# Performance work log

Hardware: AMD Instinct MI355X
Metric: run time of the kernel (lower is better)

The kernel has to match this reference:

```python
import jax, jax.numpy as jnp
import numpy as np

N_NODES = 50000
N_NEIB = 64
D = 256
BATCH = 1024
N_SAMPLES = (25, 10)  # fanout per layer (layer_specs n_sample)


def setup_inputs() -> dict:
    key = jax.random.key(0)
    ks = jax.random.split(key, 12)
    inp = {
        'ids': jax.random.randint(ks[0], (BATCH,), 0, N_NODES),
        'diff_idx': jax.random.randint(ks[1], (N_NODES, N_NEIB), 0, N_NODES),
        'diff_val': jax.random.uniform(ks[2], (N_NODES, N_NEIB), dtype=jnp.float32),
        'feats': jax.random.normal(ks[3], (N_NODES, D), dtype=jnp.float32),
    }
    # two aggregator layers, each: fc_x, fc_neib : D -> D (= output_dim//2)
    for li in range(2):
        inp[f'Wx{li+1}'] = jax.random.normal(ks[4 + 4 * li], (D, D), dtype=jnp.float32) * 0.05
        inp[f'bx{li+1}'] = jnp.zeros((D,), dtype=jnp.float32)
        inp[f'Wn{li+1}'] = jax.random.normal(ks[5 + 4 * li], (D, D), dtype=jnp.float32) * 0.05
        inp[f'bn{li+1}'] = jnp.zeros((D,), dtype=jnp.float32)
    return inp


def _sample(diff_idx, diff_val, ids, n_samples, key):
    # gather candidate neighbor rows, shared random column permutation, take first n_samples
    tmp_idx = diff_idx[ids]            # [n, N_NEIB]
    tmp_val = diff_val[ids]
    perm = jax.random.permutation(key, tmp_idx.shape[1])
    idx = tmp_idx[:, perm][:, :n_samples].reshape(-1)
    val = tmp_val[:, perm][:, :n_samples].reshape(-1)
    return idx, val


def _agg(x, neib, vals, Wx, bx, Wn, bn):
    # weighted-mean neighbor aggregation + self/neib linear combine + relu
    n = x.shape[0]
    d = neib.shape[1]
    neib = neib.reshape(n, -1, d)              # [n, s, d]
    vals = vals.reshape(n, -1)                 # [n, s]
    w = vals / (jnp.sum(vals, axis=1, keepdims=True) + 1e-10)
    m = jnp.einsum('nsd,ns->nd', neib, w)      # weighted mean of neighbors
    return jax.nn.relu(x @ Wx + bx + m @ Wn + bn)


def reference(ids, diff_idx, diff_val, feats,
              Wx1, bx1, Wn1, bn1, Wx2, bx2, Wn2, bn2):
    skey = jax.random.key(42)
    all_feats = [feats[ids]]
    all_vals = []
    cur = ids
    for li, n in enumerate(N_SAMPLES):
        cur, vals = _sample(diff_idx, diff_val, cur, n, jax.random.fold_in(skey, li))
        all_feats.append(feats[cur])
        all_vals.append(vals)
    params = [(Wx1, bx1, Wn1, bn1), (Wx2, bx2, Wn2, bn2)]
    for Wx, bx, Wn, bn in params:
        all_feats = [_agg(all_feats[k], all_feats[k + 1], all_vals[k], Wx, bx, Wn, bn)
                     for k in range(len(all_feats) - 1)]
    assert len(all_feats) == 1
    return all_feats[0]  # [BATCH, D]
```

## Files before the change

### kernel.cpp

```cpp
#include <hip/hip_runtime.h>
#include <stdint.h>
#include <stddef.h>
#include <algorithm>

#define BATCH  1024
#define S1     25
#define S2     10
#define DIM    256
#define NNEIB  64
#define L2ROWS (BATCH * S1)
#define MROWS  (BATCH + BATCH * S1)
#define KTOT   512
#define NFEAT  50000

struct Perm25 { int p[S1]; };
struct Perm10 { int p[S2]; };

typedef __attribute__((ext_vector_type(8))) short short8;
typedef __attribute__((ext_vector_type(4))) float f32x4;

static inline uint32_t rotl_(uint32_t x, int d) { return (x << d) | (x >> (32 - d)); }

static void tf2x32(uint32_t k0, uint32_t k1, uint32_t x0, uint32_t x1,
                   uint32_t* o0, uint32_t* o1) {
  const uint32_t ks0 = k0, ks1 = k1, ks2 = k0 ^ k1 ^ 0x1BD11BDAu;
  static const int R[8] = {13, 15, 26, 6, 17, 29, 16, 24};
  x0 += ks0; x1 += ks1;
  for (int g = 0; g < 5; ++g) {
    const int* rr = R + (g & 1) * 4;
    for (int i = 0; i < 4; i++) { x0 += x1; x1 = rotl_(x1, rr[i]); x1 ^= x0; }
    uint32_t a, b;
    switch (g) {
      default:
      case 0: a = ks1; b = ks2; break;
      case 1: a = ks2; b = ks0; break;
      case 2: a = ks0; b = ks1; break;
      case 3: a = ks1; b = ks2; break;
      case 4: a = ks2; b = ks0; break;
    }
    x0 += a; x1 = x1 + b + (uint32_t)(g + 1);
  }
  *o0 = x0; *o1 = x1;
}

static void compute_perm(uint32_t li, int n, int* out) {
  uint32_t k0, k1, s0, s1;
  tf2x32(0u, 42u, 0u, li, &k0, &k1);
  tf2x32(k0, k1, 0u, 1u, &s0, &s1);
  uint32_t bits[NNEIB];
  for (int i = 0; i < NNEIB; i++) {
    uint32_t a, b;
    tf2x32(s0, s1, 0u, (uint32_t)i, &a, &b);
    bits[i] = a ^ b;
  }
  int idx[NNEIB];
  for (int i = 0; i < NNEIB; i++) idx[i] = i;
  std::stable_sort(idx, idx + NNEIB, [&](int A, int B) { return bits[A] < bits[B]; });
  for (int j = 0; j < n; j++) out[j] = idx[j];
}

__device__ __forceinline__ unsigned short f2bf(float x) {
  union { float f; uint32_t u; } v; v.f = x;
  uint32_t r = (v.u + 0x7FFFu + ((v.u >> 16) & 1u)) >> 16;
  return (unsigned short)r;
}
__device__ __forceinline__ float bfbits2f(uint32_t lo16) {
  union { uint32_t u; float f; } v; v.u = lo16 << 16;
  return v.f;
}
__device__ __forceinline__ void gload16(const unsigned short* g, unsigned short* l) {
  __builtin_amdgcn_global_load_lds(
      (const __attribute__((address_space(1))) unsigned int*)g,
      (__attribute__((address_space(3))) unsigned int*)l, 16, 0, 0);
}


#define PREP_CONVF   12500
#define PREP_CONVW   512
#define PREP_BLOCKS  (PREP_CONVF + 2 * PREP_CONVW + 4)
__global__ __launch_bounds__(256) void prep_k(
    const float* __restrict__ feats, uint32_t* __restrict__ fb,
    const float* __restrict__ Wx1, const float* __restrict__ Wn1,
    unsigned short* __restrict__ Wt1,
    const float* __restrict__ Wx2, const float* __restrict__ Wn2,
    unsigned short* __restrict__ Wt2,
    const int* __restrict__ ids, const int* __restrict__ dix,
    const float* __restrict__ dval, int* __restrict__ idx1,
    float* __restrict__ w1, Perm25 pm) {
  int b = blockIdx.x, t = threadIdx.x;
  if (b < PREP_CONVF) {
    int i = b * 256 + t;
    f32x4 v = *(const f32x4*)&feats[(size_t)i * 4];
    uint2 o;
    o.x = f2bf(v.x) | ((uint32_t)f2bf(v.y) << 16);
    o.y = f2bf(v.z) | ((uint32_t)f2bf(v.w) << 16);
    ((uint2*)fb)[i] = o;
  } else if (b < PREP_CONVF + 2 * PREP_CONVW) {
    int wi = b - PREP_CONVF;
    const float* Wx = (wi < PREP_CONVW) ? Wx1 : Wx2;
    const float* Wn = (wi < PREP_CONVW) ? Wn1 : Wn2;
    unsigned short* Wt = (wi < PREP_CONVW) ? Wt1 : Wt2;
    int idx = (wi % PREP_CONVW) * 256 + t;
    int n = idx >> 9, k = idx & 511;
    float v = (k < DIM) ? Wx[(size_t)k * DIM + n] : Wn[(size_t)(k - DIM) * DIM + n];
    Wt[(size_t)n * KTOT + k] = f2bf(v);
  } else {
    int i = (b - PREP_CONVF - 2 * PREP_CONVW) * 256 + t;
    if (i >= BATCH) return;
    int nid = ids[i];
    const float* vr = dval + (size_t)nid * NNEIB;
    const int* ir = dix + (size_t)nid * NNEIB;
    float v[S1];
    float s = 0.f;
    for (int j = 0; j < S1; j++) { v[j] = vr[pm.p[j]]; s += v[j]; }
    float inv = 1.f / (s + 1e-10f);
    for (int j = 0; j < S1; j++) {
      w1[i * S1 + j] = v[j] * inv;
      idx1[i * S1 + j] = ir[pm.p[j]];
    }
  }
}

template <int S>
__device__ __forceinline__ void agg_pairs(const uint4* __restrict__ fb, int nbl,
                                          float wl, int lane, float a[8]) {
  int h = lane >> 5, l5 = lane & 31;
#pragma unroll
  for (int p = 0; p < (S + 1) / 2; p++) {
    int jj = 2 * p + h;
    int nid = __shfl(nbl, (jj < S) ? jj : 0);
    float wj = (jj < S) ? __shfl(wl, jj) : 0.f;
    uint4 u = fb[(size_t)nid * 32 + l5];
    a[0] += wj * bfbits2f(u.x & 0xffffu); a[1] += wj * bfbits2f(u.x >> 16);
    a[2] += wj * bfbits2f(u.y & 0xffffu); a[3] += wj * bfbits2f(u.y >> 16);
    a[4] += wj * bfbits2f(u.z & 0xffffu); a[5] += wj * bfbits2f(u.z >> 16);
    a[6] += wj * bfbits2f(u.w & 0xffffu); a[7] += wj * bfbits2f(u.w >> 16);
  }
}

__global__ __launch_bounds__(256) void stage1_k(
    const uint4* __restrict__ fb, const int* __restrict__ idx1,
    const float* __restrict__ w1, const int* __restrict__ dix,
    const float* __restrict__ dval, Perm10 pm2, uint4* __restrict__ M1) {
  int wave = threadIdx.x >> 6, lane = threadIdx.x & 63;
  int r = blockIdx.x * 4 + wave;
  float a[8] = {0.f, 0.f, 0.f, 0.f, 0.f, 0.f, 0.f, 0.f};
  if (r < BATCH) {
    int nbl = 0; float wl = 0.f;
    if (lane < S1) { nbl = idx1[r * S1 + lane]; wl = w1[r * S1 + lane]; }
    agg_pairs<S1>(fb, nbl, wl, lane, a);
  } else {
    int nx = idx1[r - BATCH];
    int nbl = 0; float vj = 0.f;
    if (lane < S2) {
      int c = pm2.p[lane];
      nbl = dix[(size_t)nx * NNEIB + c];
      vj = dval[(size_t)nx * NNEIB + c];
    }
    float tot = 0.f;
#pragma unroll
    for (int j = 0; j < S2; j++) tot += __shfl(vj, j);
    float wl = vj / (tot + 1e-10f);
    agg_pairs<S2>(fb, nbl, wl, lane, a);
  }
#pragma unroll
  for (int q = 0; q < 8; q++) a[q] += __shfl_xor(a[q], 32);
  if (lane < 32) {
    uint4 o;
    o.x = f2bf(a[0]) | ((uint32_t)f2bf(a[1]) << 16);
    o.y = f2bf(a[2]) | ((uint32_t)f2bf(a[3]) << 16);
    o.z = f2bf(a[4]) | ((uint32_t)f2bf(a[5]) << 16);
    o.w = f2bf(a[6]) | ((uint32_t)f2bf(a[7]) << 16);
    M1[(size_t)r * 32 + (lane & 31)] = o;
  }
}

__global__ __launch_bounds__(256) void stage2_k(
    const uint2* __restrict__ Hb, const float* __restrict__ w1,
    uint2* __restrict__ M2) {
  int wave = threadIdx.x >> 6, lane = threadIdx.x & 63;
  int i = blockIdx.x * 4 + wave;
  float wl = (lane < S1) ? w1[(size_t)i * S1 + lane] : 0.f;
  const uint2* hb = Hb + (size_t)(BATCH + i * S1) * 64 + lane;
  float a0 = 0.f, a1 = 0.f, a2 = 0.f, a3 = 0.f;
#pragma unroll
  for (int j = 0; j < S1; j++) {
    float wj = __shfl(wl, j);
    uint2 u = hb[(size_t)j * 64];
    a0 += wj * bfbits2f(u.x & 0xffffu);
    a1 += wj * bfbits2f(u.x >> 16);
    a2 += wj * bfbits2f(u.y & 0xffffu);
    a3 += wj * bfbits2f(u.y >> 16);
  }
  uint2 o;
  o.x = f2bf(a0) | ((uint32_t)f2bf(a1) << 16);
  o.y = f2bf(a2) | ((uint32_t)f2bf(a3) << 16);
  M2[(size_t)i * 64 + lane] = o;
}

#define BK 32
template <int TBM, int TBN, bool OUT_BF16, bool GATHER>
__global__ __launch_bounds__(256) void gemm_k(
    const unsigned short* __restrict__ Ax, const int* __restrict__ ids,
    const int* __restrict__ idx1, const unsigned short* __restrict__ Am,
    const unsigned short* __restrict__ Wt, const float* __restrict__ bx,
    const float* __restrict__ bn, void* __restrict__ OutP) {
  constexpr int MI = TBM / 32;
  constexpr int NJ = TBN / 32;
  __shared__ __align__(16) unsigned short As[TBM][BK];
  __shared__ __align__(16) unsigned short Bs[TBN][BK];
  int t = threadIdx.x;
  int wave = t >> 6, lane = t & 63, quad = lane >> 4, l16 = lane & 15;
  int wm = (wave >> 1) * (TBM / 2);
  int wn = (wave & 1) * (TBN / 2);
  int row0 = blockIdx.x * TBM, col0 = blockIdx.y * TBN;

  f32x4 acc[MI][NJ];
#pragma unroll
  for (int i = 0; i < MI; i++)
#pragma unroll
    for (int j = 0; j < NJ; j++) acc[i][j] = (f32x4){0.f, 0.f, 0.f, 0.f};

  int rl = lane >> 2;
  int cl = (lane & 3) * 8;

  const unsigned short* xsrc[TBM / 64];
  const unsigned short* msrc[TBM / 64];
#pragma unroll
  for (int c = 0; c < TBM / 64; c++) {
    int grow = row0 + c * 64 + wave * 16 + rl;
    int xr = GATHER ? ((grow < BATCH) ? ids[grow] : idx1[grow - BATCH]) : grow;
    xsrc[c] = Ax + (size_t)xr * DIM + cl;
    msrc[c] = Am + (size_t)grow * DIM + cl - DIM;
  }

  for (int k0 = 0; k0 < KTOT; k0 += BK) {
#pragma unroll
    for (int c = 0; c < TBM / 64; c++)
      gload16(((k0 < DIM) ? xsrc[c] : msrc[c]) + k0, &As[c * 64 + wave * 16][0]);
#pragma unroll
    for (int c = 0; c < TBN / 64; c++) {
      int row = c * 64 + wave * 16 + rl;
      gload16(Wt + (size_t)(col0 + row) * KTOT + k0 + cl, &Bs[c * 64 + wave * 16][0]);
    }
    __syncthreads();

    short8 af[MI], bfr[NJ];
#pragma unroll
    for (int i = 0; i < MI; i++)
      af[i] = *(const short8*)&As[wm + i * 16 + l16][quad * 8];
#pragma unroll
    for (int j = 0; j < NJ; j++)
      bfr[j] = *(const short8*)&Bs[wn + j * 16 + l16][quad * 8];
#pragma unroll
    for (int i = 0; i < MI; i++)
#pragma unroll
      for (int j = 0; j < NJ; j++)
        acc[i][j] = __builtin_amdgcn_mfma_f32_16x16x32_bf16(af[i], bfr[j], acc[i][j], 0, 0, 0);
    __syncthreads();
  }

  float bias[NJ];
#pragma unroll
  for (int j = 0; j < NJ; j++) {
    int c = col0 + wn + j * 16 + l16;
    bias[j] = bx[c] + bn[c];
  }
#pragma unroll
  for (int i = 0; i < MI; i++) {
#pragma unroll
    for (int j = 0; j < NJ; j++) {
      int c = col0 + wn + j * 16 + l16;
#pragma unroll
      for (int reg = 0; reg < 4; reg++) {
        int r = row0 + wm + i * 16 + quad * 4 + reg;
        float v = fmaxf(acc[i][j][reg] + bias[j], 0.f);
        if (OUT_BF16)
          ((unsigned short*)OutP)[(size_t)r * DIM + c] = f2bf(v);
        else
          ((float*)OutP)[(size_t)r * DIM + c] = v;
      }
    }
  }
}

static inline size_t align256(size_t x) { return (x + 255) & ~(size_t)255; }

extern "C" void kernel_launch(void* const* d_in, const int* in_sizes, int n_in,
                              void* d_out, int out_size, void* d_ws, size_t ws_size,
                              hipStream_t stream) {
  const int*   ids  = (const int*)d_in[0];
  const int*   dix  = (const int*)d_in[1];
  const float* dval = (const float*)d_in[2];
  const float* feats= (const float*)d_in[3];
  const float* Wx1  = (const float*)d_in[4];
  const float* bx1  = (const float*)d_in[5];
  const float* Wn1  = (const float*)d_in[6];
  const float* bn1  = (const float*)d_in[7];
  const float* Wx2  = (const float*)d_in[8];
  const float* bx2  = (const float*)d_in[9];
  const float* Wn2  = (const float*)d_in[10];
  const float* bn2  = (const float*)d_in[11];
  float* out = (float*)d_out;

  Perm25 p25;
  Perm10 p10;
  compute_perm(0u, S1, p25.p);
  compute_perm(1u, S2, p10.p);

  char* w = (char*)d_ws;
  int*            idx1 = (int*)w;            w += align256(sizeof(int) * L2ROWS);
  float*          w1   = (float*)w;          w += align256(sizeof(float) * L2ROWS);
  uint32_t*       fb   = (uint32_t*)w;       w += align256(2 * (size_t)NFEAT * DIM);
  unsigned short* M1   = (unsigned short*)w; w += align256(2 * (size_t)MROWS * DIM);
  unsigned short* Hb   = (unsigned short*)w; w += align256(2 * (size_t)MROWS * DIM);
  unsigned short* M2   = (unsigned short*)w; w += align256(2 * (size_t)BATCH * DIM);
  unsigned short* Wt1  = (unsigned short*)w; w += align256(2 * (size_t)DIM * KTOT);
  unsigned short* Wt2  = (unsigned short*)w; w += align256(2 * (size_t)DIM * KTOT);

  prep_k<<<PREP_BLOCKS, 256, 0, stream>>>(feats, fb, Wx1, Wn1, Wt1, Wx2, Wn2, Wt2,
                                          ids, dix, dval, idx1, w1, p25);
  stage1_k<<<MROWS / 4, 256, 0, stream>>>((const uint4*)fb, idx1, w1, dix, dval, p10,
                                          (uint4*)M1);
  gemm_k<128, 128, true, true><<<dim3(MROWS / 128, DIM / 128), 256, 0, stream>>>(
      (const unsigned short*)fb, ids, idx1, M1, Wt1, bx1, bn1, Hb);
  stage2_k<<<BATCH / 4, 256, 0, stream>>>((const uint2*)Hb, w1, (uint2*)M2);
  gemm_k<64, 64, false, false><<<dim3(BATCH / 64, DIM / 64), 256, 0, stream>>>(
      Hb, nullptr, nullptr, M2, Wt2, bx2, bn2, out);
}
```

Measured before the change: 183.1 us.

## Add dedicated layer-1 GEMM with 64x128 tiles, BK=64 and XOR-swizzled LDS

Replaces the generic templated GEMM for the large first-layer matmul with a specialised kernel. It uses 64x128 tiles, which doubles the grid and improves fill of the GPU's compute units. It also uses a K step of 64 (two MFMAs per tile pair), which halves the number of barrier iterations. An XOR swizzle on the LDS column layout is meant to avoid bank conflicts on the fragment reads. The layer-2 GEMM is simplified to a non-gather fp32-output specialisation, and the smaller tile raises B-matrix reload traffic per output.

```diff
diff --git a/kernel.cpp b/kernel.cpp
--- a/kernel.cpp
+++ b/kernel.cpp
@@ -198,13 +198,104 @@
   M2[(size_t)i * 64 + lane] = o;
 }
 
+__global__ __launch_bounds__(256, 4) void gemm1_k(
+    const unsigned short* __restrict__ fb, const int* __restrict__ ids,
+    const int* __restrict__ idx1, const unsigned short* __restrict__ M1,
+    const unsigned short* __restrict__ Wt, const float* __restrict__ bx,
+    const float* __restrict__ bn, unsigned short* __restrict__ Hb) {
+  __shared__ __align__(16) unsigned short As[64][64];
+  __shared__ __align__(16) unsigned short Bs[128][64];
+  int t = threadIdx.x;
+  int wave = t >> 6, lane = t & 63, quad = lane >> 4, l16 = lane & 15;
+  int wm = (wave >> 1) * 32;
+  int wn = (wave & 1) * 64;
+  int row0 = blockIdx.x * 64, col0 = blockIdx.y * 128;
+
+  f32x4 acc[2][4];
+#pragma unroll
+  for (int i = 0; i < 2; i++)
+#pragma unroll
+    for (int j = 0; j < 4; j++) acc[i][j] = (f32x4){0.f, 0.f, 0.f, 0.f};
+
+  int lrow = lane >> 3;
+  int scol = (((lane & 7) ^ (lrow & 7)) << 3);
+
+  const unsigned short* xsA[2];
+  const unsigned short* msA[2];
+#pragma unroll
+  for (int cc = 0; cc < 2; cc++) {
+    int grow = row0 + (wave * 2 + cc) * 8 + lrow;
+    int xr = (grow < BATCH) ? ids[grow] : idx1[grow - BATCH];
+    xsA[cc] = fb + (size_t)xr * DIM + scol;
+    msA[cc] = M1 + (size_t)grow * DIM + scol - DIM;
+  }
+  const unsigned short* bsrc[4];
+#pragma unroll
+  for (int cc = 0; cc < 4; cc++) {
+    int brow = col0 + (wave * 4 + cc) * 8 + lrow;
+    bsrc[cc] = Wt + (size_t)brow * KTOT + scol;
+  }
+
+  for (int k0 = 0; k0 < KTOT; k0 += 64) {
+#pragma unroll
+    for (int cc = 0; cc < 2; cc++)
+      gload16(((k0 < DIM) ? xsA[cc] : msA[cc]) + k0, &As[(wave * 2 + cc) * 8][0]);
+#pragma unroll
+    for (int cc = 0; cc < 4; cc++)
+      gload16(bsrc[cc] + k0, &Bs[(wave * 4 + cc) * 8][0]);
+    __syncthreads();
+
+    short8 af[2][2], bf8[4][2];
+#pragma unroll
+    for (int i = 0; i < 2; i++)
+#pragma unroll
+      for (int kk = 0; kk < 2; kk++)
+        af[i][kk] = *(const short8*)
+            &As[wm + i * 16 + l16][(((kk << 2) + quad) ^ (l16 & 7)) << 3];
+#pragma unroll
+    for (int j = 0; j < 4; j++)
+#pragma unroll
+      for (int kk = 0; kk < 2; kk++)
+        bf8[j][kk] = *(const short8*)
+            &Bs[wn + j * 16 + l16][(((kk << 2) + quad) ^ (l16 & 7)) << 3];
+#pragma unroll
+    for (int i = 0; i < 2; i++)
+#pragma unroll
+      for (int j = 0; j < 4; j++)
+#pragma unroll
+        for (int kk = 0; kk < 2; kk++)
+          acc[i][j] = __builtin_amdgcn_mfma_f32_16x16x32_bf16(
+              af[i][kk], bf8[j][kk], acc[i][j], 0, 0, 0);
+    __syncthreads();
+  }
+
+  float bias[4];
+#pragma unroll
+  for (int j = 0; j < 4; j++) {
+    int c = col0 + wn + j * 16 + l16;
+    bias[j] = bx[c] + bn[c];
+  }
+#pragma unroll
+  for (int i = 0; i < 2; i++) {
+#pragma unroll
+    for (int j = 0; j < 4; j++) {
+      int c = col0 + wn + j * 16 + l16;
+#pragma unroll
+      for (int reg = 0; reg < 4; reg++) {
+        int r = row0 + wm + i * 16 + quad * 4 + reg;
+        float v = fmaxf(acc[i][j][reg] + bias[j], 0.f);
+        Hb[(size_t)r * DIM + c] = f2bf(v);
+      }
+    }
+  }
+}
+
 #define BK 32
-template <int TBM, int TBN, bool OUT_BF16, bool GATHER>
-__global__ __launch_bounds__(256) void gemm_k(
-    const unsigned short* __restrict__ Ax, const int* __restrict__ ids,
-    const int* __restrict__ idx1, const unsigned short* __restrict__ Am,
+template <int TBM, int TBN>
+__global__ __launch_bounds__(256) void gemm2_k(
+    const unsigned short* __restrict__ Ax, const unsigned short* __restrict__ Am,
     const unsigned short* __restrict__ Wt, const float* __restrict__ bx,
-    const float* __restrict__ bn, void* __restrict__ OutP) {
+    const float* __restrict__ bn, float* __restrict__ Out) {
   constexpr int MI = TBM / 32;
   constexpr int NJ = TBN / 32;
   __shared__ __align__(16) unsigned short As[TBM][BK];
@@ -229,8 +320,7 @@
 #pragma unroll
   for (int c = 0; c < TBM / 64; c++) {
     int grow = row0 + c * 64 + wave * 16 + rl;
-    int xr = GATHER ? ((grow < BATCH) ? ids[grow] : idx1[grow - BATCH]) : grow;
-    xsrc[c] = Ax + (size_t)xr * DIM + cl;
+    xsrc[c] = Ax + (size_t)grow * DIM + cl;
     msrc[c] = Am + (size_t)grow * DIM + cl - DIM;
   }
 
@@ -274,11 +364,7 @@
 #pragma unroll
       for (int reg = 0; reg < 4; reg++) {
         int r = row0 + wm + i * 16 + quad * 4 + reg;
-        float v = fmaxf(acc[i][j][reg] + bias[j], 0.f);
-        if (OUT_BF16)
-          ((unsigned short*)OutP)[(size_t)r * DIM + c] = f2bf(v);
-        else
-          ((float*)OutP)[(size_t)r * DIM + c] = v;
+        Out[(size_t)r * DIM + c] = fmaxf(acc[i][j][reg] + bias[j], 0.f);
       }
     }
   }
@@ -322,9 +408,9 @@
                                           ids, dix, dval, idx1, w1, p25);
   stage1_k<<<MROWS / 4, 256, 0, stream>>>((const uint4*)fb, idx1, w1, dix, dval, p10,
                                           (uint4*)M1);
-  gemm_k<128, 128, true, true><<<dim3(MROWS / 128, DIM / 128), 256, 0, stream>>>(
+  gemm1_k<<<dim3(MROWS / 64, DIM / 128), 256, 0, stream>>>(
       (const unsigned short*)fb, ids, idx1, M1, Wt1, bx1, bn1, Hb);
   stage2_k<<<BATCH / 4, 256, 0, stream>>>((const uint2*)Hb, w1, (uint2*)M2);
-  gemm_k<64, 64, false, false><<<dim3(BATCH / 64, DIM / 64), 256, 0, stream>>>(
-      Hb, nullptr, nullptr, M2, Wt2, bx2, bn2, out);
-}
+  gemm2_k<64, 64><<<dim3(BATCH / 64, DIM / 64), 256, 0, stream>>>(
+      Hb, M2, Wt2, bx2, bn2, out);
+}
```

Measured after the change: 179.7 us (median of 2 runs). Within noise of the previous version (-1.9%).

## Double-buffer GEMM shared tiles with XOR swizzle and BK=64, 64x128 tiles

Applied to the files above, without the earlier changes.

Rewrites the bf16 MFMA GEMM to use double-buffered shared memory, so the next K-tile's loads are issued before computing on the current one. This removes one barrier per iteration. K-step grows to 64 with an XOR-swizzled column layout to avoid LDS bank conflicts, and both GEMMs now use a 64x128 block tile with a launch-bounds occupancy hint. The layer-1 grid gets more blocks, at the cost of more shared memory per block and a different tile shape for the small second GEMM.

```diff
diff --git a/kernel.cpp b/kernel.cpp
--- a/kernel.cpp
+++ b/kernel.cpp
@@ -198,78 +198,96 @@
   M2[(size_t)i * 64 + lane] = o;
 }
 
-#define BK 32
-template <int TBM, int TBN, bool OUT_BF16, bool GATHER>
-__global__ __launch_bounds__(256) void gemm_k(
+template <bool GATHER, bool OUT_BF16>
+__global__ __launch_bounds__(256, 4) void gemm_k(
     const unsigned short* __restrict__ Ax, const int* __restrict__ ids,
     const int* __restrict__ idx1, const unsigned short* __restrict__ Am,
     const unsigned short* __restrict__ Wt, const float* __restrict__ bx,
     const float* __restrict__ bn, void* __restrict__ OutP) {
-  constexpr int MI = TBM / 32;
-  constexpr int NJ = TBN / 32;
-  __shared__ __align__(16) unsigned short As[TBM][BK];
-  __shared__ __align__(16) unsigned short Bs[TBN][BK];
+  __shared__ __align__(16) unsigned short As[2][64][64];
+  __shared__ __align__(16) unsigned short Bs[2][128][64];
   int t = threadIdx.x;
   int wave = t >> 6, lane = t & 63, quad = lane >> 4, l16 = lane & 15;
-  int wm = (wave >> 1) * (TBM / 2);
-  int wn = (wave & 1) * (TBN / 2);
-  int row0 = blockIdx.x * TBM, col0 = blockIdx.y * TBN;
-
-  f32x4 acc[MI][NJ];
-#pragma unroll
-  for (int i = 0; i < MI; i++)
-#pragma unroll
-    for (int j = 0; j < NJ; j++) acc[i][j] = (f32x4){0.f, 0.f, 0.f, 0.f};
-
-  int rl = lane >> 2;
-  int cl = (lane & 3) * 8;
-
-  const unsigned short* xsrc[TBM / 64];
-  const unsigned short* msrc[TBM / 64];
-#pragma unroll
-  for (int c = 0; c < TBM / 64; c++) {
-    int grow = row0 + c * 64 + wave * 16 + rl;
+  int wm = (wave >> 1) * 32;
+  int wn = (wave & 1) * 64;
+  int row0 = blockIdx.x * 64, col0 = blockIdx.y * 128;
+
+  f32x4 acc[2][4];
+#pragma unroll
+  for (int i = 0; i < 2; i++)
+#pragma unroll
+    for (int j = 0; j < 4; j++) acc[i][j] = (f32x4){0.f, 0.f, 0.f, 0.f};
+
+  int lrow = lane >> 3;
+  int scol = (((lane & 7) ^ (lrow & 7)) << 3);
+
+  const unsigned short* xsA[2];
+  const unsigned short* msA[2];
+#pragma unroll
+  for (int cc = 0; cc < 2; cc++) {
+    int grow = row0 + (wave * 2 + cc) * 8 + lrow;
     int xr = GATHER ? ((grow < BATCH) ? ids[grow] : idx1[grow - BATCH]) : grow;
-    xsrc[c] = Ax + (size_t)xr * DIM + cl;
-    msrc[c] = Am + (size_t)grow * DIM + cl - DIM;
-  }
-
-  for (int k0 = 0; k0 < KTOT; k0 += BK) {
-#pragma unroll
-    for (int c = 0; c < TBM / 64; c++)
-      gload16(((k0 < DIM) ? xsrc[c] : msrc[c]) + k0, &As[c * 64 + wave * 16][0]);
-#pragma unroll
-    for (int c = 0; c < TBN / 64; c++) {
-      int row = c * 64 + wave * 16 + rl;
-      gload16(Wt + (size_t)(col0 + row) * KTOT + k0 + cl, &Bs[c * 64 + wave * 16][0]);
-    }
+    xsA[cc] = Ax + (size_t)xr * DIM + scol;
+    msA[cc] = Am + (size_t)grow * DIM + scol - DIM;
+  }
+  const unsigned short* bsrc[4];
+#pragma unroll
+  for (int cc = 0; cc < 4; cc++) {
+    int brow = col0 + (wave * 4 + cc) * 8 + lrow;
+    bsrc[cc] = Wt + (size_t)brow * KTOT + scol;
+  }
+
+  auto stage = [&](int buf, int k0) {
+#pragma unroll
+    for (int cc = 0; cc < 2; cc++)
+      gload16(((k0 < DIM) ? xsA[cc] : msA[cc]) + k0, &As[buf][(wave * 2 + cc) * 8][0]);
+#pragma unroll
+    for (int cc = 0; cc < 4; cc++)
+      gload16(bsrc[cc] + k0, &Bs[buf][(wave * 4 + cc) * 8][0]);
+  };
+
+  stage(0, 0);
+  __syncthreads();
+
+  int cur = 0;
+  for (int k0 = 0; k0 < KTOT; k0 += 64, cur ^= 1) {
+    if (k0 + 64 < KTOT) stage(cur ^ 1, k0 + 64);
+
+    short8 af[2][2], bf8[4][2];
+#pragma unroll
+    for (int i = 0; i < 2; i++)
+#pragma unroll
+      for (int kk = 0; kk < 2; kk++)
+        af[i][kk] = *(const short8*)
+            &As[cur][wm + i * 16 + l16][(((kk << 2) + quad) ^ (l16 & 7)) << 3];
+#pragma unroll
+    for (int j = 0; j < 4; j++)
+#pragma unroll
+      for (int kk = 0; kk < 2; kk++)
+        bf8[j][kk] = *(const short8*)
+            &Bs[cur][wn + j * 16 + l16][(((kk << 2) + quad) ^ (l16 & 7)) << 3];
+#pragma unroll
+    for (int i = 0; i < 2; i++)
+#pragma unroll
+      for (int j = 0; j < 4; j++)
+#pragma unroll
+        for (int kk = 0; kk < 2; kk++)
+          acc[i][j] = __builtin_amdgcn_mfma_f32_16x16x32_bf16(
+              af[i][kk], bf8[j][kk], acc[i][j], 0, 0, 0);
+
     __syncthreads();
-
-    short8 af[MI], bfr[NJ];
-#pragma unroll
-    for (int i = 0; i < MI; i++)
-      af[i] = *(const short8*)&As[wm + i * 16 + l16][quad * 8];
-#pragma unroll
-    for (int j = 0; j < NJ; j++)
-      bfr[j] = *(const short8*)&Bs[wn + j * 16 + l16][quad * 8];
-#pragma unroll
-    for (int i = 0; i < MI; i++)
-#pragma unroll
-      for (int j = 0; j < NJ; j++)
-        acc[i][j] = __builtin_amdgcn_mfma_f32_16x16x32_bf16(af[i], bfr[j], acc[i][j], 0, 0, 0);
-    __syncthreads();
-  }
-
-  float bias[NJ];
-#pragma unroll
-  for (int j = 0; j < NJ; j++) {
+  }
+
+  float bias[4];
+#pragma unroll
+  for (int j = 0; j < 4; j++) {
     int c = col0 + wn + j * 16 + l16;
     bias[j] = bx[c] + bn[c];
   }
 #pragma unroll
-  for (int i = 0; i < MI; i++) {
-#pragma unroll
-    for (int j = 0; j < NJ; j++) {
+  for (int i = 0; i < 2; i++) {
+#pragma unroll
+    for (int j = 0; j < 4; j++) {
       int c = col0 + wn + j * 16 + l16;
 #pragma unroll
       for (int reg = 0; reg < 4; reg++) {
@@ -322,9 +340,9 @@
                                           ids, dix, dval, idx1, w1, p25);
   stage1_k<<<MROWS / 4, 256, 0, stream>>>((const uint4*)fb, idx1, w1, dix, dval, p10,
                                           (uint4*)M1);
-  gemm_k<128, 128, true, true><<<dim3(MROWS / 128, DIM / 128), 256, 0, stream>>>(
+  gemm_k<true, true><<<dim3(MROWS / 64, DIM / 128), 256, 0, stream>>>(
       (const unsigned short*)fb, ids, idx1, M1, Wt1, bx1, bn1, Hb);
   stage2_k<<<BATCH / 4, 256, 0, stream>>>((const uint2*)Hb, w1, (uint2*)M2);
-  gemm_k<64, 64, false, false><<<dim3(BATCH / 64, DIM / 64), 256, 0, stream>>>(
+  gemm_k<false, false><<<dim3(BATCH / 64, DIM / 128), 256, 0, stream>>>(
       Hb, nullptr, nullptr, M2, Wt2, bx2, bn2, out);
 }
```

New measurement: 184.5 us. Within noise of the previous version (+0.8%).
